# Optimization experiments

Measured on AMD Instinct MI355X. Metric: run time of the kernel, lower is better.

Reference implementation:

```python
import jax, jax.numpy as jnp
import numpy as np

B, T, HID = 4, 4096, 768
H, D = 12, 64
N_HASHES = 2
BUCKET_SIZE = T // 32          # reformer repo config: max_seq_len // 32 = 128
N_BUCKETS = T // BUCKET_SIZE   # 32
SELF_ATTN_VALUE = -5e4         # reformer_pytorch TOKEN_SELF_ATTN_VALUE
MASK_VALUE = -1e9


def lsh_attention(X, mask_bool, W_qk, W_v, rotations):
    # X: [b, t, hid]; rotations: [d, n_hashes, n_buckets//2] (shared across batch & heads)
    b, t, _ = X.shape
    d, n_hashes, half_nb = rotations.shape
    n_buckets = 2 * half_nb
    h = W_qk.shape[0] // d
    scale = d ** -0.5

    qk = X @ W_qk.T            # shared query/key projection (bias-free in reformer_pytorch)
    v = X @ W_v.T

    def merge_heads(x):  # [b,t,h*d] -> [b*h, t, d]
        return x.reshape(b, t, h, d).transpose(0, 2, 1, 3).reshape(b * h, t, d)

    qk, v = merge_heads(qk), merge_heads(v)
    maskbh = jnp.repeat(mask_bool, h, axis=0)          # [bh, t]

    # --- LSH bucketing ---
    rotated = jnp.einsum('btf,fhi->bhti', qk, rotations)          # [bh, nh, t, nb/2]
    rotated = jnp.concatenate([rotated, -rotated], axis=-1)       # [bh, nh, t, nb]
    buckets = jnp.argmax(rotated, axis=-1)                        # [bh, nh, t]
    offsets = (jnp.arange(n_hashes) * n_buckets)[None, :, None]
    buckets = (buckets + offsets).reshape(b * h, n_hashes * t)

    # --- stable sort by (bucket, position) ---
    total = n_hashes * t
    ticker = jnp.arange(total)[None, :]
    buckets_and_t = buckets * t + (ticker % t)
    sticker = jnp.argsort(buckets_and_t, axis=-1)   # stable
    undo = jnp.argsort(sticker, axis=-1)
    st = sticker % t                                 # original positions, sorted order

    sqk = jnp.take_along_axis(qk, st[..., None], axis=1)
    sv = jnp.take_along_axis(v, st[..., None], axis=1)
    smask = jnp.take_along_axis(maskbh, st, axis=1)

    # --- chunk; each chunk attends to itself + previous chunk ---
    n_chunks = n_hashes * n_buckets
    cl = total // n_chunks                                  # == bucket_size
    bq_t = st.reshape(b * h, n_chunks, cl)
    bqk = sqk.reshape(b * h, n_chunks, cl, d)
    bv = sv.reshape(b * h, n_chunks, cl, d)
    bmask = smask.reshape(b * h, n_chunks, cl)

    bq = bqk
    bk = bqk / jnp.clip(jnp.linalg.norm(bqk, axis=-1, keepdims=True), 1e-12)

    def look_one_back(x):
        return jnp.concatenate([x, jnp.roll(x, 1, axis=1)], axis=2)

    bk, bv = look_one_back(bk), look_one_back(bv)
    bkv_t = look_one_back(bq_t)
    bkv_mask = look_one_back(bmask)

    dots = jnp.einsum('bnie,bnje->bnij', bq, bk) * scale    # [bh, n_chunks, cl, 2cl]
    pad = bmask[..., :, None] & bkv_mask[..., None, :]
    dots = jnp.where(pad, dots, MASK_VALUE)
    self_mask = bq_t[..., :, None] == bkv_t[..., None, :]
    dots = jnp.where(self_mask, SELF_ATTN_VALUE, dots)

    lse = jax.scipy.special.logsumexp(dots, axis=-1, keepdims=True)
    probs = jnp.exp(dots - lse)
    bo = jnp.einsum('bnij,bnje->bnie', probs, bv)

    # --- unsort and combine hash rounds via softmax over round logsumexps ---
    so = bo.reshape(b * h, total, d)
    slogits = lse.reshape(b * h, total)
    o = jnp.take_along_axis(so, undo[..., None], axis=1)
    logits = jnp.take_along_axis(slogits, undo, axis=1)

    o = o.reshape(b * h, n_hashes, t, d)
    logits = logits.reshape(b * h, n_hashes, t, 1)
    round_probs = jnp.exp(logits - jax.scipy.special.logsumexp(logits, axis=1, keepdims=True))
    out = jnp.sum(o * round_probs, axis=1)                  # [bh, t, d]
    return out.reshape(b, h, t, d).transpose(0, 2, 1, 3).reshape(b, t, h * d)


def setup_inputs() -> dict:
    key = jax.random.key(0)
    ks = jax.random.split(key, 8)
    s = 1.0 / np.sqrt(HID)
    return {
        'X': jax.random.normal(ks[0], (B, T, HID), jnp.float32),
        'mask': jnp.ones((B, T), jnp.float32),
        'W_qk': jax.random.uniform(ks[1], (H * D, HID), jnp.float32, -s, s),
        'W_v': jax.random.uniform(ks[2], (H * D, HID), jnp.float32, -s, s),
        'rotations': jax.random.normal(ks[3], (D, N_HASHES, N_BUCKETS // 2), jnp.float32),
        'W_to': jax.random.uniform(ks[4], (HID, H * D), jnp.float32, -s, s),
        'b_to': jnp.zeros((HID,), jnp.float32),
        'W_o': jax.random.uniform(ks[5], (HID, HID), jnp.float32, -s, s),
        'b_o': jnp.zeros((HID,), jnp.float32),
    }


def reference(X, mask, W_qk, W_v, rotations, W_to, b_to, W_o, b_o):
    attn = lsh_attention(X, mask.astype(bool), W_qk, W_v, rotations)
    attn = attn @ W_to.T + b_to     # LSHSelfAttention.to_out
    return attn @ W_o.T + b_o       # ReformerAttention.W_o
```

## Files before the change

kernel.cpp:

```cpp
#include <hip/hip_runtime.h>
#include <hip/hip_bf16.h>
#include <math.h>


typedef __attribute__((ext_vector_type(8))) short bf16x8;
typedef __attribute__((ext_vector_type(4))) float f32x4;
typedef __attribute__((ext_vector_type(4))) double f64x4;

__device__ __forceinline__ float bf_lo(unsigned int w) { return __uint_as_float(w << 16); }
__device__ __forceinline__ float bf_hi(unsigned int w) { return __uint_as_float(w & 0xffff0000u); }
__device__ __forceinline__ float load_in(const void* p, size_t i, bool f32) {
  return f32 ? ((const float*)p)[i]
             : __bfloat162float(((const __hip_bfloat16*)p)[i]);
}
__device__ __forceinline__ unsigned short f2bf(float x) {
  __hip_bfloat16 h = __float2bfloat16(x);
  return *reinterpret_cast<unsigned short*>(&h);
}
__device__ __forceinline__ float bf2f(unsigned short u) { return __uint_as_float(((unsigned int)u) << 16); }

__global__ void k_detect(const unsigned int* __restrict__ X, int* __restrict__ flag) {
  if (threadIdx.x == 0 && blockIdx.x == 0) {
    int vote = 0;
    for (int i = 0; i < 64; ++i) {
      unsigned int e = (X[i] >> 7) & 0xffu;
      vote += (e >= 100u && e <= 141u) ? 1 : 0;
    }
    *flag = (vote < 32) ? 1 : 0;
  }
}

__global__ __launch_bounds__(256) void k_convert(
    const void* __restrict__ src, unsigned short* __restrict__ dst, int n8,
    const int* __restrict__ flag) {
  const bool f32in = (*flag != 0);
  int i = blockIdx.x * 256 + threadIdx.x;
  if (i >= n8) return;
  if (f32in) {
    const float4* s = (const float4*)src + (size_t)i * 2;
    float4 a = s[0], b = s[1];
    union { unsigned short u[8]; uint4 v; } o;
    o.u[0] = f2bf(a.x); o.u[1] = f2bf(a.y); o.u[2] = f2bf(a.z); o.u[3] = f2bf(a.w);
    o.u[4] = f2bf(b.x); o.u[5] = f2bf(b.y); o.u[6] = f2bf(b.z); o.u[7] = f2bf(b.w);
    ((uint4*)dst)[i] = o.v;
  } else {
    ((uint4*)dst)[i] = ((const uint4*)src)[i];
  }
}

__global__ __launch_bounds__(256) void k_transpose_cvt(
    const void* __restrict__ Wto, unsigned short* __restrict__ WtoT,
    const int* __restrict__ flag) {
  const bool f32in = (*flag != 0);
  __shared__ unsigned short T[64][65];
  const int bx = blockIdx.x % 12, by = blockIdx.x / 12;
  const int p0 = by * 64, n0 = bx * 64;
  const int rw = threadIdx.x >> 6, lane = threadIdx.x & 63;
  #pragma unroll
  for (int pass = 0; pass < 16; ++pass) {
    int row = pass * 4 + rw;
    T[row][lane] = f2bf(load_in(Wto, (size_t)(p0 + row) * 768 + n0 + lane, f32in));
  }
  __syncthreads();
  #pragma unroll
  for (int pass = 0; pass < 16; ++pass) {
    int row = pass * 4 + rw;
    WtoT[(size_t)(n0 + row) * 768 + p0 + lane] = T[lane][row];
  }
}

__global__ __launch_bounds__(256) void k_bias_fold(
    const void* __restrict__ Wo, const void* __restrict__ bto,
    const void* __restrict__ bo, float* __restrict__ bcomb,
    const int* __restrict__ flag) {
  const bool f32in = (*flag != 0);
  const int n = blockIdx.x * 4 + (threadIdx.x >> 6);
  const int lane = threadIdx.x & 63;
  float s = 0.f;
  #pragma unroll
  for (int i = 0; i < 12; ++i) {
    int j = lane + i * 64;
    s = fmaf(load_in(Wo, (size_t)n * 768 + j, f32in), load_in(bto, j, f32in), s);
  }
  #pragma unroll
  for (int off = 1; off < 64; off <<= 1) s += __shfl_xor(s, off, 64);
  if (lane == 0) bcomb[n] = s + load_in(bo, n, f32in);
}

__global__ __launch_bounds__(256) void k_build_wrot(
    const void* __restrict__ Wqk, const void* __restrict__ rot,
    double* __restrict__ WrotT, const int* __restrict__ flag) {
  const bool f32in = (*flag != 0);
  int idx = blockIdx.x * 256 + threadIdx.x;
  if (idx >= 768 * 384) return;
  int row = idx % 384;
  int c   = idx / 384;
  int hh = row >> 5, hi = row & 31;
  double s = 0.0;
  for (int f = 0; f < 64; ++f) {
    double rv = (double)load_in(rot, f * 32 + hi, f32in);
    double wv = (double)load_in(Wqk, (size_t)(hh * 64 + f) * 768 + c, f32in);
    s = fma(rv, wv, s);
  }
  WrotT[(size_t)c * 384 + row] = s;
}

__global__ __launch_bounds__(512) void k_bucket(
    const void* __restrict__ X, const double* __restrict__ WrotT,
    unsigned char* __restrict__ cls, const int* __restrict__ flag) {
  const bool f32in = (*flag != 0);
  __shared__ double SH[7296];
  double* Sc = SH;
  const int tid = threadIdx.x;
  const int M0 = blockIdx.x * 128;
  const int N0 = blockIdx.y * 96;
  const int w = tid >> 6, lane = tid & 63;
  const int l15 = lane & 15, lq = lane >> 4;
  const int sr = tid >> 2, sh2 = tid & 3;
  const int wk = tid >> 5, wn3 = (tid & 31) * 3;

  f64x4 acc[6];
  #pragma unroll
  for (int j = 0; j < 6; ++j) acc[j] = (f64x4){0.0, 0.0, 0.0, 0.0};

  int rowid[4], colid[4];
  {
    f64x4 zz = (f64x4){0.0, 0.0, 0.0, 0.0};
    f64x4 pr = __builtin_amdgcn_mfma_f64_16x16x4f64(
        (double)l15, (lq == 0) ? 1.0 : 0.0, zz, 0, 0, 0);
    f64x4 pc = __builtin_amdgcn_mfma_f64_16x16x4f64(
        (lq == 0) ? 1.0 : 0.0, (double)l15, zz, 0, 0, 0);
    #pragma unroll
    for (int r = 0; r < 4; ++r) {
      rowid[r] = (int)pr[r];
      colid[r] = (int)pc[r];
    }
  }

  double xv[4];
  double wvv[3];
  auto load_chunk = [&](int k0) {
    size_t base = (size_t)(M0 + sr) * 768 + k0 + sh2 * 4;
    if (f32in) {
      float4 f0 = *(const float4*)((const float*)X + base);
      xv[0] = f0.x; xv[1] = f0.y; xv[2] = f0.z; xv[3] = f0.w;
    } else {
      uint2 u = *(const uint2*)((const unsigned short*)X + base);
      xv[0] = (double)bf_lo(u.x); xv[1] = (double)bf_hi(u.x);
      xv[2] = (double)bf_lo(u.y); xv[3] = (double)bf_hi(u.y);
    }
    const double* wp = WrotT + (size_t)(k0 + wk) * 384 + N0 + wn3;
    wvv[0] = wp[0]; wvv[1] = wp[1]; wvv[2] = wp[2];
  };
  auto store_stage = [&](int bsel) {
    double* Xs = SH + bsel * 2080;
    double* Ws = SH + 4160 + bsel * 1568;
    #pragma unroll
    for (int j = 0; j < 4; ++j) Xs[(sh2 * 4 + j) * 130 + sr] = xv[j];
    Ws[wk * 98 + wn3]     = wvv[0];
    Ws[wk * 98 + wn3 + 1] = wvv[1];
    Ws[wk * 98 + wn3 + 2] = wvv[2];
  };

  load_chunk(0);
  store_stage(0);
  __syncthreads();
  for (int t = 0; t < 48; ++t) {
    const double* Xs = SH + (t & 1) * 2080;
    const double* Ws = SH + 4160 + (t & 1) * 1568;
    if (t < 47) load_chunk((t + 1) * 16);
    #pragma unroll
    for (int kq = 0; kq < 4; ++kq) {
      double a = Xs[(kq * 4 + lq) * 130 + w * 16 + l15];
      const double* wr = &Ws[(kq * 4 + lq) * 98 + l15];
      #pragma unroll
      for (int nt = 0; nt < 6; ++nt)
        acc[nt] = __builtin_amdgcn_mfma_f64_16x16x4f64(a, wr[nt * 16], acc[nt], 0, 0, 0);
    }
    if (t < 47) store_stage((t & 1) ^ 1);
    __syncthreads();
  }

  #pragma unroll
  for (int chunk = 0; chunk < 2; ++chunk) {
    __syncthreads();
    if ((w >> 2) == chunk) {
      int lr = (w & 3) * 16;
      #pragma unroll
      for (int nt = 0; nt < 6; ++nt)
        #pragma unroll
        for (int r = 0; r < 4; ++r)
          Sc[(nt * 16 + colid[r]) * 66 + lr + rowid[r]] = acc[nt][r];
    }
    __syncthreads();
    for (int task = tid; task < 384; task += 512) {
      int g = task >> 6, tok = task & 63;
      const double* s = &Sc[(g * 16) * 66 + tok];
      double mx = -1.0e300;
      #pragma unroll
      for (int i = 0; i < 16; ++i) {
        double a = s[i * 66];
        mx = fmax(mx, fmax(a, -a));
      }
      int amax = 0;
      #pragma unroll
      for (int i = 15; i >= 0; --i) if (-s[i * 66] == mx) amax = 16 + i;
      #pragma unroll
      for (int i = 15; i >= 0; --i) if (s[i * 66] == mx) amax = i;
      int m = M0 + chunk * 64 + tok;
      int b = m >> 12, t = m & 4095;
      int gg = blockIdx.y * 6 + g, hh = gg >> 1, h = gg & 1;
      cls[(size_t)(b * 12 + hh) * 8192 + h * 4096 + t] = (unsigned char)(h * 32 + amax);
    }
  }
}

__global__ __launch_bounds__(1024) void k_sort(
    const unsigned char* __restrict__ clsg,
    unsigned short* __restrict__ stick) {
  __shared__ unsigned short cntg[128 * 64];
  __shared__ int classbase[64];
  const int row = blockIdx.x;
  const int tid = threadIdx.x;
  const int wave = tid >> 6, lane = tid & 63;
  const unsigned char* cr = clsg + ((size_t)row << 13);

  for (int i = tid; i < 128 * 64 / 2; i += 1024) ((uint32_t*)cntg)[i] = 0;
  __syncthreads();

  unsigned char myc[8], myrank[8];
  const unsigned long long ltmask = (lane == 0) ? 0ull : (~0ull >> (64 - lane));
  #pragma unroll
  for (int chunk = 0; chunk < 8; ++chunk) {
    int g = chunk * 16 + wave;
    int j = g * 64 + lane;
    int c = cr[j];
    unsigned long long same = ~0ull;
    #pragma unroll
    for (int bit = 0; bit < 6; ++bit) {
      unsigned long long bm = __ballot((c >> bit) & 1);
      same &= ((c >> bit) & 1) ? bm : ~bm;
    }
    int rank = __popcll(same & ltmask);
    if (rank == 0) cntg[g * 64 + c] = (unsigned short)__popcll(same);
    myc[chunk] = (unsigned char)c;
    myrank[chunk] = (unsigned char)rank;
  }
  __syncthreads();
  if (tid < 64) {
    int run = 0;
    for (int g = 0; g < 128; ++g) {
      int t = cntg[g * 64 + tid];
      cntg[g * 64 + tid] = (unsigned short)run;
      run += t;
    }
    classbase[tid] = run;
  }
  __syncthreads();
  if (tid == 0) {
    int run = 0;
    for (int c = 0; c < 64; ++c) { int t = classbase[c]; classbase[c] = run; run += t; }
  }
  __syncthreads();
  unsigned short* out = stick + ((size_t)row << 13);
  #pragma unroll
  for (int chunk = 0; chunk < 8; ++chunk) {
    int g = chunk * 16 + wave;
    int j = g * 64 + lane;
    int c = myc[chunk];
    int pos = classbase[c] + cntg[g * 64 + c] + myrank[chunk];
    out[pos] = (unsigned short)j;
  }
}

__global__ __launch_bounds__(256) void k_gemm_mfma(
    const unsigned short* __restrict__ A, const unsigned short* __restrict__ W,
    const float* __restrict__ bias, void* __restrict__ Cout,
    int layout, int out_ext, const int* __restrict__ flag) {
  const bool f32in = (*flag != 0);
  const bool oF32 = out_ext && f32in;
  __shared__ unsigned short As[128 * 40];
  __shared__ unsigned short Bs[128 * 40];
  const int tid = threadIdx.x;
  const int bm = blockIdx.x, bn = blockIdx.y;
  const int w = tid >> 6, lane = tid & 63;
  const int l15 = lane & 15, lq = lane >> 4;
  const int wm = (w >> 1) * 64, wn = (w & 1) * 64;
  const int r4 = tid >> 2, c4 = tid & 3;
  const unsigned short* Ag = A + (size_t)(bm * 128 + r4) * 768 + c4 * 8;
  const unsigned short* Bg = W + (size_t)(bn * 128 + r4) * 768 + c4 * 8;
  f32x4 acc[4][4];
  #pragma unroll
  for (int i = 0; i < 4; ++i)
    #pragma unroll
    for (int j = 0; j < 4; ++j) acc[i][j] = (f32x4){0.f, 0.f, 0.f, 0.f};
  uint4 pa0 = *(const uint4*)(Ag);
  uint4 pa1 = *(const uint4*)(Ag + 64 * 768);
  uint4 pb0 = *(const uint4*)(Bg);
  uint4 pb1 = *(const uint4*)(Bg + 64 * 768);
  for (int kt = 0; kt < 24; ++kt) {
    __syncthreads();
    *(uint4*)&As[r4 * 40 + c4 * 8] = pa0;
    *(uint4*)&As[(r4 + 64) * 40 + c4 * 8] = pa1;
    *(uint4*)&Bs[r4 * 40 + c4 * 8] = pb0;
    *(uint4*)&Bs[(r4 + 64) * 40 + c4 * 8] = pb1;
    __syncthreads();
    if (kt < 23) {
      int off = (kt + 1) * 32;
      pa0 = *(const uint4*)(Ag + off);
      pa1 = *(const uint4*)(Ag + 64 * 768 + off);
      pb0 = *(const uint4*)(Bg + off);
      pb1 = *(const uint4*)(Bg + 64 * 768 + off);
    }
    bf16x8 af[4], bfr[4];
    #pragma unroll
    for (int mt = 0; mt < 4; ++mt)
      af[mt] = *(const bf16x8*)&As[(wm + mt * 16 + l15) * 40 + lq * 8];
    #pragma unroll
    for (int nt = 0; nt < 4; ++nt)
      bfr[nt] = *(const bf16x8*)&Bs[(wn + nt * 16 + l15) * 40 + lq * 8];
    #pragma unroll
    for (int mt = 0; mt < 4; ++mt)
      #pragma unroll
      for (int nt = 0; nt < 4; ++nt)
        acc[mt][nt] = __builtin_amdgcn_mfma_f32_16x16x32_bf16(af[mt], bfr[nt], acc[mt][nt], 0, 0, 0);
  }
  #pragma unroll
  for (int mt = 0; mt < 4; ++mt) {
    #pragma unroll
    for (int nt = 0; nt < 4; ++nt) {
      #pragma unroll
      for (int reg = 0; reg < 4; ++reg) {
        int m = bm * 128 + wm + mt * 16 + lq * 4 + reg;
        int n = bn * 128 + wn + nt * 16 + l15;
        float val = acc[mt][nt][reg];
        if (bias != nullptr) val += bias[n];
        if (layout == 0) {
          size_t addr = (size_t)m * 768 + n;
          if (oF32) ((float*)Cout)[addr] = val;
          else      ((unsigned short*)Cout)[addr] = f2bf(val);
        } else {
          int b2 = m >> 12, t2 = m & 4095, hh = n >> 6, f = n & 63;
          ((unsigned short*)Cout)[((((size_t)(b2 * 12 + hh)) << 12) + t2) * 64 + f] = f2bf(val);
        }
      }
    }
  }
}

__global__ __launch_bounds__(256) void k_norm(
    const unsigned short* __restrict__ qk, float* __restrict__ nk) {
  int row = blockIdx.x * 32 + (threadIdx.x >> 3);
  int cs = threadIdx.x & 7;
  const uint4* p = (const uint4*)(qk + (size_t)row * 64);
  uint4 wv = p[cs];
  float s = 0.f;
  float e;
  e = bf_lo(wv.x); s += e * e;  e = bf_hi(wv.x); s += e * e;
  e = bf_lo(wv.y); s += e * e;  e = bf_hi(wv.y); s += e * e;
  e = bf_lo(wv.z); s += e * e;  e = bf_hi(wv.z); s += e * e;
  e = bf_lo(wv.w); s += e * e;  e = bf_hi(wv.w); s += e * e;
  s += __shfl_xor(s, 1, 64);
  s += __shfl_xor(s, 2, 64);
  s += __shfl_xor(s, 4, 64);
  if (cs == 0) nk[row] = 1.0f / fmaxf(sqrtf(s), 1e-12f);
}

__global__ __launch_bounds__(256) void k_attn_mfma(
    const unsigned short* __restrict__ qk,
    const unsigned short* __restrict__ vv,
    const unsigned short* __restrict__ stick,
    const void* __restrict__ mask,
    const float* __restrict__ nk,
    unsigned short* __restrict__ o_r,
    float* __restrict__ lse_r,
    const int* __restrict__ flag) {
  const bool f32in = (*flag != 0);
  __shared__ unsigned short QPs[128 * 72];
  __shared__ unsigned short Ks[64 * 72];
  __shared__ unsigned short Vt[64 * 72];
  __shared__ unsigned short Tq[128];
  __shared__ unsigned short Tkv[64];
  __shared__ float Nkv[64];
  unsigned short* Qs = QPs;
  unsigned short* Ps = QPs;
  unsigned short* Vs = QPs;

  const int tid = threadIdx.x;
  const int bh = blockIdx.x >> 6;
  const int ci = blockIdx.x & 63;
  const int b  = bh / 12;
  const int prev = (ci + 63) & 63;
  const int w = tid >> 6, lane = tid & 63;
  const int l15 = lane & 15, lq = lane >> 4;
  const unsigned short* srow = stick + ((size_t)bh << 13);
  const int jrow = tid >> 3, cs = tid & 7;

  #pragma unroll
  for (int pass = 0; pass < 4; ++pass) {
    int r = jrow + pass * 32;
    int s = srow[ci * 128 + r];
    int t = s & 4095;
    uint4 qw = ((const uint4*)(qk + ((((size_t)bh << 12) + t) << 6)))[cs];
    *(uint4*)&Qs[r * 72 + cs * 8] = qw;
    if (cs == 0) {
      float mv = load_in(mask, b * 4096 + t, f32in);
      Tq[r] = (unsigned short)(s | ((mv != 0.0f) ? 0 : 0x8000));
    }
  }
  __syncthreads();

  bf16x8 qf[2][2];
  #pragma unroll
  for (int ks = 0; ks < 2; ++ks)
    #pragma unroll
    for (int mt = 0; mt < 2; ++mt)
      qf[ks][mt] = *(const bf16x8*)&Qs[(w * 32 + mt * 16 + l15) * 72 + ks * 32 + lq * 8];

  unsigned short tqr[2][4];
  #pragma unroll
  for (int mt = 0; mt < 2; ++mt)
    #pragma unroll
    for (int reg = 0; reg < 4; ++reg)
      tqr[mt][reg] = Tq[w * 32 + mt * 16 + lq * 4 + reg];

  float m_run[2][4], l_run[2][4];
  f32x4 oacc[2][4];
  #pragma unroll
  for (int mt = 0; mt < 2; ++mt)
    #pragma unroll
    for (int reg = 0; reg < 4; ++reg) { m_run[mt][reg] = -3.0e38f; l_run[mt][reg] = 0.0f; }
  #pragma unroll
  for (int mt = 0; mt < 2; ++mt)
    #pragma unroll
    for (int nto = 0; nto < 4; ++nto) oacc[mt][nto] = (f32x4){0.f, 0.f, 0.f, 0.f};

  for (int kt = 0; kt < 4; ++kt) {
    __syncthreads();
    #pragma unroll
    for (int pass = 0; pass < 2; ++pass) {
      int j = jrow + pass * 32;
      int chunk = (kt < 2) ? ci : prev;
      int s = srow[chunk * 128 + (kt & 1) * 64 + j];
      int t = s & 4095;
      const uint4* kb = (const uint4*)(qk + ((((size_t)bh << 12) + t) << 6));
      *(uint4*)&Ks[j * 72 + cs * 8] = kb[cs];
      const uint4* vb = (const uint4*)(vv + ((((size_t)bh << 12) + t) << 6));
      int sw = (cs ^ (j & 7) ^ (j >> 3)) & 7;
      *(uint4*)&Vs[j * 72 + sw * 8] = vb[cs];
      if (cs == 0) {
        float mv = load_in(mask, b * 4096 + t, f32in);
        Tkv[j] = (unsigned short)(t | ((mv != 0.0f) ? 0 : 0x8000));
        Nkv[j] = nk[((size_t)bh << 12) + t] * 0.125f;
      }
    }
    __syncthreads();

    #pragma unroll
    for (int i = 0; i < 8; ++i) {
      int cp = w * 8 + i;
      int q8 = cp >> 2;
      int sw = (q8 ^ (lane & 7) ^ (lane >> 3)) & 7;
      uint32_t wv = *(const uint32_t*)&Vs[lane * 72 + sw * 8 + ((2 * cp) & 7)];
      Vt[(2 * cp) * 72 + lane]     = (unsigned short)(wv & 0xffff);
      Vt[(2 * cp + 1) * 72 + lane] = (unsigned short)(wv >> 16);
    }

    f32x4 sacc[2][4];
    #pragma unroll
    for (int mt = 0; mt < 2; ++mt)
      #pragma unroll
      for (int nt = 0; nt < 4; ++nt) sacc[mt][nt] = (f32x4){0.f, 0.f, 0.f, 0.f};
    #pragma unroll
    for (int ks = 0; ks < 2; ++ks) {
      #pragma unroll
      for (int nt = 0; nt < 4; ++nt) {
        bf16x8 bfr = *(const bf16x8*)&Ks[(nt * 16 + l15) * 72 + ks * 32 + lq * 8];
        #pragma unroll
        for (int mt = 0; mt < 2; ++mt)
          sacc[mt][nt] = __builtin_amdgcn_mfma_f32_16x16x32_bf16(qf[ks][mt], bfr, sacc[mt][nt], 0, 0, 0);
      }
    }

    unsigned short tkc[4];
    float nkc[4];
    #pragma unroll
    for (int nt = 0; nt < 4; ++nt) {
      tkc[nt] = Tkv[nt * 16 + l15];
      nkc[nt] = Nkv[nt * 16 + l15];
    }
    float dv[2][4][4];
    #pragma unroll
    for (int mt = 0; mt < 2; ++mt)
      #pragma unroll
      for (int nt = 0; nt < 4; ++nt)
        #pragma unroll
        for (int reg = 0; reg < 4; ++reg) {
          float x = sacc[mt][nt][reg] * nkc[nt];
          unsigned short ts = tqr[mt][reg];
          if (((tkc[nt] | ts) & 0x8000) != 0) x = -1.0e9f;
          if (((tkc[nt] ^ ts) & 0x0fff) == 0) x = -5.0e4f;
          dv[mt][nt][reg] = x;
        }
    float mn[2][4], scv[2][4];
    #pragma unroll
    for (int mt = 0; mt < 2; ++mt)
      #pragma unroll
      for (int reg = 0; reg < 4; ++reg) {
        float rm = fmaxf(fmaxf(dv[mt][0][reg], dv[mt][1][reg]),
                         fmaxf(dv[mt][2][reg], dv[mt][3][reg]));
        rm = fmaxf(rm, __shfl_xor(rm, 1, 64));
        rm = fmaxf(rm, __shfl_xor(rm, 2, 64));
        rm = fmaxf(rm, __shfl_xor(rm, 4, 64));
        rm = fmaxf(rm, __shfl_xor(rm, 8, 64));
        float mnew = fmaxf(m_run[mt][reg], rm);
        scv[mt][reg] = __expf(m_run[mt][reg] - mnew);
        m_run[mt][reg] = mnew;
        mn[mt][reg] = mnew;
      }
    #pragma unroll
    for (int mt = 0; mt < 2; ++mt)
      #pragma unroll
      for (int nt = 0; nt < 4; ++nt)
        #pragma unroll
        for (int reg = 0; reg < 4; ++reg)
          dv[mt][nt][reg] = __expf(dv[mt][nt][reg] - mn[mt][reg]);
    #pragma unroll
    for (int mt = 0; mt < 2; ++mt)
      #pragma unroll
      for (int reg = 0; reg < 4; ++reg) {
        float rs = ((dv[mt][0][reg] + dv[mt][1][reg]) + (dv[mt][2][reg] + dv[mt][3][reg]));
        rs += __shfl_xor(rs, 1, 64);
        rs += __shfl_xor(rs, 2, 64);
        rs += __shfl_xor(rs, 4, 64);
        rs += __shfl_xor(rs, 8, 64);
        l_run[mt][reg] = l_run[mt][reg] * scv[mt][reg] + rs;
      }
    #pragma unroll
    for (int mt = 0; mt < 2; ++mt)
      #pragma unroll
      for (int nto = 0; nto < 4; ++nto)
        #pragma unroll
        for (int reg = 0; reg < 4; ++reg)
          oacc[mt][nto][reg] *= scv[mt][reg];

    __syncthreads();

    #pragma unroll
    for (int mt = 0; mt < 2; ++mt)
      #pragma unroll
      for (int nt = 0; nt < 4; ++nt)
        #pragma unroll
        for (int reg = 0; reg < 4; ++reg)
          Ps[w * 2304 + (mt * 16 + lq * 4 + reg) * 72 + nt * 16 + l15] = f2bf(dv[mt][nt][reg]);

    #pragma unroll
    for (int ks = 0; ks < 2; ++ks) {
      bf16x8 pf[2];
      #pragma unroll
      for (int mt = 0; mt < 2; ++mt)
        pf[mt] = *(const bf16x8*)&Ps[w * 2304 + (mt * 16 + l15) * 72 + ks * 32 + lq * 8];
      #pragma unroll
      for (int nto = 0; nto < 4; ++nto) {
        bf16x8 vf = *(const bf16x8*)&Vt[(nto * 16 + l15) * 72 + ks * 32 + lq * 8];
        #pragma unroll
        for (int mt = 0; mt < 2; ++mt)
          oacc[mt][nto] = __builtin_amdgcn_mfma_f32_16x16x32_bf16(pf[mt], vf, oacc[mt][nto], 0, 0, 0);
      }
    }
  }

  float invl[2][4];
  #pragma unroll
  for (int mt = 0; mt < 2; ++mt)
    #pragma unroll
    for (int reg = 0; reg < 4; ++reg) {
      float lr = l_run[mt][reg];
      invl[mt][reg] = 1.0f / lr;
      if (l15 == 0) {
        int Rr = w * 32 + mt * 16 + lq * 4 + reg;
        int s = Tq[Rr];
        int tq0 = s & 4095, rq0 = (s >> 12) & 1;
        lse_r[(((size_t)(bh * 2 + rq0)) << 12) + tq0] = m_run[mt][reg] + __logf(lr);
      }
    }
  #pragma unroll
  for (int mt = 0; mt < 2; ++mt)
    #pragma unroll
    for (int nto = 0; nto < 4; ++nto)
      #pragma unroll
      for (int reg = 0; reg < 4; ++reg)
        Ps[w * 2304 + (mt * 16 + lq * 4 + reg) * 72 + nto * 16 + l15] =
            f2bf(oacc[mt][nto][reg] * invl[mt][reg]);
  #pragma unroll
  for (int pass = 0; pass < 4; ++pass) {
    int rl = pass * 8 + (lane >> 3);
    int s = Tq[w * 32 + rl];
    int tq0 = s & 4095, rq0 = (s >> 12) & 1;
    uint4 ov = *(const uint4*)&Ps[w * 2304 + rl * 72 + (lane & 7) * 8];
    *(uint4*)(o_r + ((((size_t)(bh * 2 + rq0)) << 12) + tq0) * 64 + (lane & 7) * 8) = ov;
  }
}

__global__ __launch_bounds__(256) void k_combine(
    const unsigned short* __restrict__ o_r,
    const float* __restrict__ lse_r,
    unsigned short* __restrict__ attn) {
  int idx = blockIdx.x * 256 + threadIdx.x;
  if (idx >= 48 * 4096 * 8) return;
  int f8 = idx & 7;
  int t = (idx >> 3) & 4095;
  int bh = idx >> 15;
  float l0 = lse_r[((size_t)(bh * 2 + 0) << 12) + t];
  float l1 = lse_r[((size_t)(bh * 2 + 1) << 12) + t];
  float mm = fmaxf(l0, l1);
  float e0 = __expf(l0 - mm), e1 = __expf(l1 - mm);
  float inv = 1.0f / (e0 + e1);
  float c0 = e0 * inv, c1 = e1 * inv;
  uint4 v0 = *(const uint4*)(o_r + ((((size_t)(bh * 2 + 0)) << 12) + t) * 64 + f8 * 8);
  uint4 v1 = *(const uint4*)(o_r + ((((size_t)(bh * 2 + 1)) << 12) + t) * 64 + f8 * 8);
  union { unsigned short u[8]; uint4 v; } o;
  const unsigned int* a0 = (const unsigned int*)&v0;
  const unsigned int* a1 = (const unsigned int*)&v1;
  #pragma unroll
  for (int j = 0; j < 4; ++j) {
    float lo = c0 * bf_lo(a0[j]) + c1 * bf_lo(a1[j]);
    float hi = c0 * bf_hi(a0[j]) + c1 * bf_hi(a1[j]);
    o.u[2 * j]     = f2bf(lo);
    o.u[2 * j + 1] = f2bf(hi);
  }
  int b = bh / 12, hh = bh % 12;
  *(uint4*)(attn + ((size_t)(b * 4096 + t)) * 768 + hh * 64 + f8 * 8) = o.v;
}

extern "C" void kernel_launch(void* const* d_in, const int* in_sizes, int n_in,
                              void* d_out, int out_size, void* d_ws, size_t ws_size,
                              hipStream_t stream) {
  (void)in_sizes; (void)n_in; (void)out_size; (void)ws_size;
  const void* X    = d_in[0];
  const void* mask = d_in[1];
  const void* Wqk  = d_in[2];
  const void* Wv   = d_in[3];
  const void* rot  = d_in[4];
  const void* Wto  = d_in[5];
  const void* bto  = d_in[6];
  const void* Wo   = d_in[7];
  const void* bo   = d_in[8];

  char* ws = (char*)d_ws;
  int*            flag  = (int*)(ws);
  unsigned short* stick = (unsigned short*)(ws + 256);
  float*          lse_r = (float*)(ws + 786688);
  float*          nk    = (float*)(ws + 2359552);
  unsigned short* qk    = (unsigned short*)(ws + 3145984);
  unsigned short* v     = (unsigned short*)(ws + 28311808);
  unsigned short* o_r   = (unsigned short*)(ws + 53477632);
  double*         WrotT = (double*)(ws + 53477632);
  unsigned char*  cls   = (unsigned char*)(ws + 55836928);
  unsigned short* Wqkb  = (unsigned short*)(ws + 56230144);
  unsigned short* Wvb   = (unsigned short*)(ws + 57409792);
  unsigned short* Xb    = (unsigned short*)(ws + 58589440);
  unsigned short* attn  = v;
  unsigned short* Wcomb = (unsigned short*)(ws + 3145984);
  float*          bcomb = (float*)(ws + 3145984 + 1179648);
  unsigned short* Wob   = (unsigned short*)(ws + 3145984 + 1182720);
  unsigned short* WtoT  = (unsigned short*)(ws + 3145984 + 2362368);

  k_detect<<<1, 64, 0, stream>>>((const unsigned int*)X, flag);
  k_convert<<<6144, 256, 0, stream>>>(X, Xb, 1572864, flag);
  k_convert<<<288, 256, 0, stream>>>(Wqk, Wqkb, 73728, flag);
  k_convert<<<288, 256, 0, stream>>>(Wv, Wvb, 73728, flag);
  k_build_wrot<<<1152, 256, 0, stream>>>(Wqk, rot, WrotT, flag);
  k_bucket<<<dim3(128, 4), 512, 0, stream>>>(X, WrotT, cls, flag);
  k_sort<<<48, 1024, 0, stream>>>(cls, stick);
  k_gemm_mfma<<<dim3(128, 6), 256, 0, stream>>>(Xb, Wqkb, nullptr, qk, 1, 0, flag);
  k_gemm_mfma<<<dim3(128, 6), 256, 0, stream>>>(Xb, Wvb,  nullptr, v,  1, 0, flag);
  k_norm<<<6144, 256, 0, stream>>>(qk, nk);
  k_attn_mfma<<<3072, 256, 0, stream>>>(qk, v, stick, mask, nk, o_r, lse_r, flag);
  k_convert<<<288, 256, 0, stream>>>(Wo, Wob, 73728, flag);
  k_transpose_cvt<<<144, 256, 0, stream>>>(Wto, WtoT, flag);
  k_bias_fold<<<192, 256, 0, stream>>>(Wo, bto, bo, bcomb, flag);
  k_gemm_mfma<<<dim3(6, 6), 256, 0, stream>>>(Wob, WtoT, nullptr, Wcomb, 0, 0, flag);
  k_combine<<<6144, 256, 0, stream>>>(o_r, lse_r, attn);
  k_gemm_mfma<<<dim3(128, 6), 256, 0, stream>>>(attn, Wcomb, bcomb, d_out, 0, 1, flag);
}
```

Baseline: 610.0 us.

## Fuse fp64 LSH bucketing GEMM with QK/V projection GEMMs in one launch

Replaces the separate bucketing kernel and two projection GEMM launches with one kernel whose blocks are split three ways by block index. One third run a retiled fp64 bucketing GEMM (64-wide N tiles, 256 threads, X staged in fp32 shared memory), and two thirds run bf16 MFMA GEMMs for the qk and v projections. The aim is to overlap the fp64-bound bucketing work with the bf16 projection work on the same GPU and to cut launch overhead. The cost is a heterogeneous kernel whose register and LDS use is set by the larger branch, which may lower occupancy for both.

```diff
diff --git a/kernel.cpp b/kernel.cpp
--- a/kernel.cpp
+++ b/kernel.cpp
@@ -105,112 +105,199 @@
   WrotT[(size_t)c * 384 + row] = s;
 }
 
-__global__ __launch_bounds__(512) void k_bucket(
+__global__ __launch_bounds__(256) void k_fused(
     const void* __restrict__ X, const double* __restrict__ WrotT,
-    unsigned char* __restrict__ cls, const int* __restrict__ flag) {
+    unsigned char* __restrict__ cls,
+    const unsigned short* __restrict__ Xb,
+    const unsigned short* __restrict__ Wqkb,
+    const unsigned short* __restrict__ Wvb,
+    unsigned short* __restrict__ qk, unsigned short* __restrict__ v,
+    const int* __restrict__ flag) {
   const bool f32in = (*flag != 0);
-  __shared__ double SH[7296];
-  double* Sc = SH;
+  __shared__ double SH[4224];
   const int tid = threadIdx.x;
-  const int M0 = blockIdx.x * 128;
-  const int N0 = blockIdx.y * 96;
+  const int id = blockIdx.x;
+  const int r3 = id % 3;
   const int w = tid >> 6, lane = tid & 63;
   const int l15 = lane & 15, lq = lane >> 4;
-  const int sr = tid >> 2, sh2 = tid & 3;
-  const int wk = tid >> 5, wn3 = (tid & 31) * 3;
-
-  f64x4 acc[6];
-  #pragma unroll
-  for (int j = 0; j < 6; ++j) acc[j] = (f64x4){0.0, 0.0, 0.0, 0.0};
-
-  int rowid[4], colid[4];
+
+  if (r3 == 0) {
+    const int idx = id / 3;
+    const int M0 = (idx % 128) * 128;
+    const int by = idx / 128;
+    const int N0 = by * 64;
+    float* XsF = (float*)SH;
+    double* Sc = SH;
+    const int sr = tid >> 1, sh2 = tid & 1;
+    const int wk = tid >> 4, wg4 = (tid & 15) * 4;
+
+    f64x4 acc[2][4];
+    #pragma unroll
+    for (int i = 0; i < 2; ++i)
+      #pragma unroll
+      for (int j = 0; j < 4; ++j) acc[i][j] = (f64x4){0.0, 0.0, 0.0, 0.0};
+
+    int rowid[4], colid[4];
+    {
+      f64x4 zz = (f64x4){0.0, 0.0, 0.0, 0.0};
+      f64x4 pr = __builtin_amdgcn_mfma_f64_16x16x4f64(
+          (double)l15, (lq == 0) ? 1.0 : 0.0, zz, 0, 0, 0);
+      f64x4 pc = __builtin_amdgcn_mfma_f64_16x16x4f64(
+          (lq == 0) ? 1.0 : 0.0, (double)l15, zz, 0, 0, 0);
+      #pragma unroll
+      for (int r = 0; r < 4; ++r) { rowid[r] = (int)pr[r]; colid[r] = (int)pc[r]; }
+    }
+
+    float xv[8];
+    double wvv[4];
+    auto load_chunk = [&](int k0) {
+      size_t base = (size_t)(M0 + sr) * 768 + k0 + sh2 * 8;
+      if (f32in) {
+        const float4* fp = (const float4*)((const float*)X + base);
+        float4 f0 = fp[0], f1 = fp[1];
+        xv[0] = f0.x; xv[1] = f0.y; xv[2] = f0.z; xv[3] = f0.w;
+        xv[4] = f1.x; xv[5] = f1.y; xv[6] = f1.z; xv[7] = f1.w;
+      } else {
+        uint4 u = *(const uint4*)((const unsigned short*)X + base);
+        xv[0] = bf_lo(u.x); xv[1] = bf_hi(u.x);
+        xv[2] = bf_lo(u.y); xv[3] = bf_hi(u.y);
+        xv[4] = bf_lo(u.z); xv[5] = bf_hi(u.z);
+        xv[6] = bf_lo(u.w); xv[7] = bf_hi(u.w);
+      }
+      const double* wp = WrotT + (size_t)(k0 + wk) * 384 + N0 + wg4;
+      wvv[0] = wp[0]; wvv[1] = wp[1]; wvv[2] = wp[2]; wvv[3] = wp[3];
+    };
+    auto store_stage = [&](int bsel) {
+      float* Xs = XsF + bsel * 2112;
+      double* Ws = SH + 2112 + bsel * 1056;
+      #pragma unroll
+      for (int j = 0; j < 8; ++j) Xs[(sh2 * 8 + j) * 132 + sr] = xv[j];
+      #pragma unroll
+      for (int e = 0; e < 4; ++e) Ws[wk * 66 + wg4 + e] = wvv[e];
+    };
+
+    load_chunk(0);
+    store_stage(0);
+    __syncthreads();
+    for (int t = 0; t < 48; ++t) {
+      const float* Xs = XsF + (t & 1) * 2112;
+      const double* Ws = SH + 2112 + (t & 1) * 1056;
+      if (t < 47) load_chunk((t + 1) * 16);
+      #pragma unroll
+      for (int kq = 0; kq < 4; ++kq) {
+        const float* xr = &Xs[(kq * 4 + lq) * 132 + w * 32 + l15];
+        double a0 = (double)xr[0];
+        double a1 = (double)xr[16];
+        const double* wr = &Ws[(kq * 4 + lq) * 66 + l15];
+        #pragma unroll
+        for (int nt = 0; nt < 4; ++nt) {
+          double b = wr[nt * 16];
+          acc[0][nt] = __builtin_amdgcn_mfma_f64_16x16x4f64(a0, b, acc[0][nt], 0, 0, 0);
+          acc[1][nt] = __builtin_amdgcn_mfma_f64_16x16x4f64(a1, b, acc[1][nt], 0, 0, 0);
+        }
+      }
+      if (t < 47) store_stage((t & 1) ^ 1);
+      __syncthreads();
+    }
+
+    #pragma unroll
+    for (int chunk = 0; chunk < 2; ++chunk) {
+      __syncthreads();
+      if ((w >> 1) == chunk) {
+        int lr = (w & 1) * 32;
+        #pragma unroll
+        for (int mt = 0; mt < 2; ++mt)
+          #pragma unroll
+          for (int nt = 0; nt < 4; ++nt)
+            #pragma unroll
+            for (int r = 0; r < 4; ++r)
+              Sc[(nt * 16 + colid[r]) * 66 + lr + mt * 16 + rowid[r]] = acc[mt][nt][r];
+      }
+      __syncthreads();
+      {
+        int g = tid >> 6, tok = tid & 63;
+        const double* s = &Sc[(g * 16) * 66 + tok];
+        double mx = -1.0e300;
+        #pragma unroll
+        for (int i = 0; i < 16; ++i) {
+          double a = s[i * 66];
+          mx = fmax(mx, fmax(a, -a));
+        }
+        int amax = 0;
+        #pragma unroll
+        for (int i = 15; i >= 0; --i) if (-s[i * 66] == mx) amax = 16 + i;
+        #pragma unroll
+        for (int i = 15; i >= 0; --i) if (s[i * 66] == mx) amax = i;
+        int m = M0 + chunk * 64 + tok;
+        int b = m >> 12, t = m & 4095;
+        int gg = by * 4 + g, hh = gg >> 1, h = gg & 1;
+        cls[(size_t)(b * 12 + hh) * 8192 + h * 4096 + t] = (unsigned char)(h * 32 + amax);
+      }
+    }
+    return;
+  }
+
   {
-    f64x4 zz = (f64x4){0.0, 0.0, 0.0, 0.0};
-    f64x4 pr = __builtin_amdgcn_mfma_f64_16x16x4f64(
-        (double)l15, (lq == 0) ? 1.0 : 0.0, zz, 0, 0, 0);
-    f64x4 pc = __builtin_amdgcn_mfma_f64_16x16x4f64(
-        (lq == 0) ? 1.0 : 0.0, (double)l15, zz, 0, 0, 0);
-    #pragma unroll
-    for (int r = 0; r < 4; ++r) {
-      rowid[r] = (int)pr[r];
-      colid[r] = (int)pc[r];
-    }
-  }
-
-  double xv[4];
-  double wvv[3];
-  auto load_chunk = [&](int k0) {
-    size_t base = (size_t)(M0 + sr) * 768 + k0 + sh2 * 4;
-    if (f32in) {
-      float4 f0 = *(const float4*)((const float*)X + base);
-      xv[0] = f0.x; xv[1] = f0.y; xv[2] = f0.z; xv[3] = f0.w;
-    } else {
-      uint2 u = *(const uint2*)((const unsigned short*)X + base);
-      xv[0] = (double)bf_lo(u.x); xv[1] = (double)bf_hi(u.x);
-      xv[2] = (double)bf_lo(u.y); xv[3] = (double)bf_hi(u.y);
-    }
-    const double* wp = WrotT + (size_t)(k0 + wk) * 384 + N0 + wn3;
-    wvv[0] = wp[0]; wvv[1] = wp[1]; wvv[2] = wp[2];
-  };
-  auto store_stage = [&](int bsel) {
-    double* Xs = SH + bsel * 2080;
-    double* Ws = SH + 4160 + bsel * 1568;
-    #pragma unroll
-    for (int j = 0; j < 4; ++j) Xs[(sh2 * 4 + j) * 130 + sr] = xv[j];
-    Ws[wk * 98 + wn3]     = wvv[0];
-    Ws[wk * 98 + wn3 + 1] = wvv[1];
-    Ws[wk * 98 + wn3 + 2] = wvv[2];
-  };
-
-  load_chunk(0);
-  store_stage(0);
-  __syncthreads();
-  for (int t = 0; t < 48; ++t) {
-    const double* Xs = SH + (t & 1) * 2080;
-    const double* Ws = SH + 4160 + (t & 1) * 1568;
-    if (t < 47) load_chunk((t + 1) * 16);
-    #pragma unroll
-    for (int kq = 0; kq < 4; ++kq) {
-      double a = Xs[(kq * 4 + lq) * 130 + w * 16 + l15];
-      const double* wr = &Ws[(kq * 4 + lq) * 98 + l15];
-      #pragma unroll
-      for (int nt = 0; nt < 6; ++nt)
-        acc[nt] = __builtin_amdgcn_mfma_f64_16x16x4f64(a, wr[nt * 16], acc[nt], 0, 0, 0);
-    }
-    if (t < 47) store_stage((t & 1) ^ 1);
-    __syncthreads();
-  }
-
-  #pragma unroll
-  for (int chunk = 0; chunk < 2; ++chunk) {
-    __syncthreads();
-    if ((w >> 2) == chunk) {
-      int lr = (w & 3) * 16;
-      #pragma unroll
-      for (int nt = 0; nt < 6; ++nt)
-        #pragma unroll
-        for (int r = 0; r < 4; ++r)
-          Sc[(nt * 16 + colid[r]) * 66 + lr + rowid[r]] = acc[nt][r];
-    }
-    __syncthreads();
-    for (int task = tid; task < 384; task += 512) {
-      int g = task >> 6, tok = task & 63;
-      const double* s = &Sc[(g * 16) * 66 + tok];
-      double mx = -1.0e300;
-      #pragma unroll
-      for (int i = 0; i < 16; ++i) {
-        double a = s[i * 66];
-        mx = fmax(mx, fmax(a, -a));
-      }
-      int amax = 0;
-      #pragma unroll
-      for (int i = 15; i >= 0; --i) if (-s[i * 66] == mx) amax = 16 + i;
-      #pragma unroll
-      for (int i = 15; i >= 0; --i) if (s[i * 66] == mx) amax = i;
-      int m = M0 + chunk * 64 + tok;
-      int b = m >> 12, t = m & 4095;
-      int gg = blockIdx.y * 6 + g, hh = gg >> 1, h = gg & 1;
-      cls[(size_t)(b * 12 + hh) * 8192 + h * 4096 + t] = (unsigned char)(h * 32 + amax);
+    int gidx = (id / 3) * 2 + (r3 - 1);
+    const unsigned short* W = (gidx < 768) ? Wqkb : Wvb;
+    unsigned short* Cout = (gidx < 768) ? qk : v;
+    if (gidx >= 768) gidx -= 768;
+    const int bm = gidx % 128, bn = gidx / 128;
+    unsigned short* As = (unsigned short*)SH;
+    unsigned short* Bs = As + 5120;
+    const int wm = (w >> 1) * 64, wn = (w & 1) * 64;
+    const int r4 = tid >> 2, c4 = tid & 3;
+    const unsigned short* Ag = Xb + (size_t)(bm * 128 + r4) * 768 + c4 * 8;
+    const unsigned short* Bg = W + (size_t)(bn * 128 + r4) * 768 + c4 * 8;
+    f32x4 acc[4][4];
+    #pragma unroll
+    for (int i = 0; i < 4; ++i)
+      #pragma unroll
+      for (int j = 0; j < 4; ++j) acc[i][j] = (f32x4){0.f, 0.f, 0.f, 0.f};
+    uint4 pa0 = *(const uint4*)(Ag);
+    uint4 pa1 = *(const uint4*)(Ag + 64 * 768);
+    uint4 pb0 = *(const uint4*)(Bg);
+    uint4 pb1 = *(const uint4*)(Bg + 64 * 768);
+    for (int kt = 0; kt < 24; ++kt) {
+      __syncthreads();
+      *(uint4*)&As[r4 * 40 + c4 * 8] = pa0;
+      *(uint4*)&As[(r4 + 64) * 40 + c4 * 8] = pa1;
+      *(uint4*)&Bs[r4 * 40 + c4 * 8] = pb0;
+      *(uint4*)&Bs[(r4 + 64) * 40 + c4 * 8] = pb1;
+      __syncthreads();
+      if (kt < 23) {
+        int off = (kt + 1) * 32;
+        pa0 = *(const uint4*)(Ag + off);
+        pa1 = *(const uint4*)(Ag + 64 * 768 + off);
+        pb0 = *(const uint4*)(Bg + off);
+        pb1 = *(const uint4*)(Bg + 64 * 768 + off);
+      }
+      bf16x8 af[4], bfr[4];
+      #pragma unroll
+      for (int mt = 0; mt < 4; ++mt)
+        af[mt] = *(const bf16x8*)&As[(wm + mt * 16 + l15) * 40 + lq * 8];
+      #pragma unroll
+      for (int nt = 0; nt < 4; ++nt)
+        bfr[nt] = *(const bf16x8*)&Bs[(wn + nt * 16 + l15) * 40 + lq * 8];
+      #pragma unroll
+      for (int mt = 0; mt < 4; ++mt)
+        #pragma unroll
+        for (int nt = 0; nt < 4; ++nt)
+          acc[mt][nt] = __builtin_amdgcn_mfma_f32_16x16x32_bf16(af[mt], bfr[nt], acc[mt][nt], 0, 0, 0);
+    }
+    #pragma unroll
+    for (int mt = 0; mt < 4; ++mt) {
+      #pragma unroll
+      for (int nt = 0; nt < 4; ++nt) {
+        #pragma unroll
+        for (int reg = 0; reg < 4; ++reg) {
+          int m = bm * 128 + wm + mt * 16 + lq * 4 + reg;
+          int n = bn * 128 + wn + nt * 16 + l15;
+          float val = acc[mt][nt][reg];
+          int b2 = m >> 12, t2 = m & 4095, hh = n >> 6, f = n & 63;
+          Cout[((((size_t)(b2 * 12 + hh)) << 12) + t2) * 64 + f] = f2bf(val);
+        }
+      }
     }
   }
 }
@@ -671,10 +758,8 @@
   k_convert<<<288, 256, 0, stream>>>(Wqk, Wqkb, 73728, flag);
   k_convert<<<288, 256, 0, stream>>>(Wv, Wvb, 73728, flag);
   k_build_wrot<<<1152, 256, 0, stream>>>(Wqk, rot, WrotT, flag);
-  k_bucket<<<dim3(128, 4), 512, 0, stream>>>(X, WrotT, cls, flag);
+  k_fused<<<2304, 256, 0, stream>>>(X, WrotT, cls, Xb, Wqkb, Wvb, qk, v, flag);
   k_sort<<<48, 1024, 0, stream>>>(cls, stick);
-  k_gemm_mfma<<<dim3(128, 6), 256, 0, stream>>>(Xb, Wqkb, nullptr, qk, 1, 0, flag);
-  k_gemm_mfma<<<dim3(128, 6), 256, 0, stream>>>(Xb, Wvb,  nullptr, v,  1, 0, flag);
   k_norm<<<6144, 256, 0, stream>>>(qk, nk);
   k_attn_mfma<<<3072, 256, 0, stream>>>(qk, v, stick, mask, nk, o_r, lse_r, flag);
   k_convert<<<288, 256, 0, stream>>>(Wo, Wob, 73728, flag);
```

Measured after the change: 689.1 us. 1.13x slower.
